# Kernel optimization log

Hardware: AMD Instinct MI355X
Metric: run time of the kernel (lower is better)

Reference implementation:

```python
import jax, jax.numpy as jnp
import numpy as np

NUM_CLASSES = 80
IMG = 640
STRIDES = (8, 16, 32)
CENTER_RADIUS = 2.5
TOPK = 10  # n_candidate_k; dynamic_ks = clamp(int(sum top-10 IoU), 1) <= 10


def _make_grids():
    gs, ss = [], []
    for s in STRIDES:
        n = IMG // s
        gy, gx = np.meshgrid(np.arange(n), np.arange(n), indexing="ij")
        gs.append(np.stack([gx.ravel(), gy.ravel()], 1).astype(np.float32))
        ss.append(np.full(n * n, s, np.float32))
    return np.concatenate(gs, 0), np.concatenate(ss, 0)


def setup_inputs() -> dict:
    key = jax.random.key(0)
    B, T, C = 16, 128, NUM_CLASSES
    grid_np, stride_np = _make_grids()
    A = grid_np.shape[0]  # 8400
    k1, k2, k3, k4, k5, k6 = jax.random.split(key, 6)
    # pred boxes: plausible abs xyxy around anchor centers
    ctr = jnp.asarray((grid_np + 0.5) * stride_np[:, None])[None]
    ctr = ctr + 4.0 * jax.random.normal(k1, (B, A, 2))
    wh = jnp.asarray(stride_np)[None, :, None] * jax.random.uniform(k2, (B, A, 2), minval=1.0, maxval=4.0)
    box = jnp.concatenate([ctr - wh / 2, ctr + wh / 2], -1)
    logits = 2.0 * jax.random.normal(k3, (B, A, 1 + C))
    pred = jnp.concatenate([box, logits], -1)  # [B, A, 5+C]
    # targets: [B, T, 6] = (batch_id, cid, x1, y1, x2, y2)
    tc = jax.random.uniform(k4, (B, T, 2), minval=60.0, maxval=580.0)
    twh = jax.random.uniform(k5, (B, T, 2), minval=30.0, maxval=200.0)
    tbox = jnp.concatenate([tc - twh / 2, tc + twh / 2], -1)
    cid = jax.random.randint(k6, (B, T, 1), 0, C).astype(jnp.float32)
    bid = jnp.broadcast_to(jnp.arange(B, dtype=jnp.float32)[:, None, None], (B, T, 1))
    target = jnp.concatenate([bid, cid, tbox], -1)
    return {"pred": pred, "target": target,
            "grid_mask": jnp.asarray(grid_np), "stride_mask": jnp.asarray(stride_np)}


def _pairwise_iou(a, b):
    # a [T,4], b [A,4], xyxy -> [T,A]
    lt = jnp.maximum(a[:, None, :2], b[None, :, :2])
    rb = jnp.minimum(a[:, None, 2:], b[None, :, 2:])
    wh = jnp.clip(rb - lt, 0.0, None)
    inter = wh[..., 0] * wh[..., 1]
    area_a = jnp.clip(a[:, 2] - a[:, 0], 0.0, None) * jnp.clip(a[:, 3] - a[:, 1], 0.0, None)
    area_b = jnp.clip(b[:, 2] - b[:, 0], 0.0, None) * jnp.clip(b[:, 3] - b[:, 1], 0.0, None)
    return inter / (area_a[:, None] + area_b[None, :] - inter + 1e-8)


def _ciou(p, t):
    # complete IoU, elementwise over leading dims, xyxy
    lt = jnp.maximum(p[..., :2], t[..., :2])
    rb = jnp.minimum(p[..., 2:], t[..., 2:])
    wh = jnp.clip(rb - lt, 0.0, None)
    inter = wh[..., 0] * wh[..., 1]
    wp, hp = p[..., 2] - p[..., 0], p[..., 3] - p[..., 1]
    wt, ht = t[..., 2] - t[..., 0], t[..., 3] - t[..., 1]
    iou = inter / (wp * hp + wt * ht - inter + 1e-8)
    cwh = jnp.maximum(p[..., 2:], t[..., 2:]) - jnp.minimum(p[..., :2], t[..., :2])
    c2 = cwh[..., 0] ** 2 + cwh[..., 1] ** 2 + 1e-8
    rho2 = (((p[..., 0] + p[..., 2]) - (t[..., 0] + t[..., 2])) ** 2
            + ((p[..., 1] + p[..., 3]) - (t[..., 1] + t[..., 3])) ** 2) / 4.0
    v = (4.0 / jnp.pi ** 2) * (jnp.arctan(wt / (ht + 1e-8)) - jnp.arctan(wp / (hp + 1e-8))) ** 2
    alpha = v / (1.0 - iou + v + 1e-8)
    return iou - rho2 / c2 - alpha * v


def _bce_logits(x, t):
    return jnp.maximum(x, 0.0) - x * t + jnp.log1p(jnp.exp(-jnp.abs(x)))


def _assign_image(pred_i, tgt_i, grid, stride):
    # pred_i [A,5+C], tgt_i [T,6]
    A, T, C = pred_i.shape[0], tgt_i.shape[0], NUM_CLASSES
    tbox = tgt_i[:, 2:6]
    cid = tgt_i[:, 1].astype(jnp.int32)
    xc = (grid[:, 0] + 0.5) * stride  # [A]
    yc = (grid[:, 1] + 0.5) * stride
    d = jnp.stack([xc[None] - tbox[:, 0:1], yc[None] - tbox[:, 1:2],
                   tbox[:, 2:3] - xc[None], tbox[:, 3:4] - yc[None]], -1)  # [T,A,4]
    in_boxes = d.min(-1) > 0.0  # [T,A]
    txc = (tbox[:, 0] + tbox[:, 2]) / 2
    tyc = (tbox[:, 1] + tbox[:, 3]) / 2
    in_centers = jnp.maximum(jnp.abs(xc[None] - txc[:, None]),
                             jnp.abs(yc[None] - tyc[:, None])) < CENTER_RADIUS * stride[None]
    in_box = in_boxes.any(0) | in_centers.any(0)  # [A], candidate anchors
    in_box_center = in_boxes & in_centers  # [T,A]
    iou = jnp.where(in_box[None], _pairwise_iou(tbox, pred_i[:, :4]), 0.0)  # [T,A]
    iou_cost = -jnp.log(iou + 1e-8)
    prob = jnp.sqrt(jax.nn.sigmoid(pred_i[:, 4:5]) * jax.nn.sigmoid(pred_i[:, 5:]))  # [A,C]
    logp = jnp.maximum(jnp.log(prob), -100.0)      # torch BCE clamps log at -100
    log1mp = jnp.maximum(jnp.log1p(-prob), -100.0)
    # sum_c BCE(prob, onehot(cid)) computed analytically (avoids [T,A,C]):
    cls_cost = -(log1mp.sum(-1)[None, :] + (logp - log1mp)[:, cid].T)  # [T,A]
    # 1e9 keeps anchors outside in_box out of the candidate pool (original slices them away)
    cost = cls_cost + 3.0 * iou_cost + 1e5 * (~in_box_center) + 1e9 * (~in_box)[None, :]
    topk_ious, _ = jax.lax.top_k(iou, TOPK)  # [T,10]
    dyn_k = jnp.maximum(topk_ious.sum(1).astype(jnp.int32), 1)  # [T]
    _, idx = jax.lax.top_k(-cost, TOPK)  # 10 lowest-cost anchors per target
    sel = jnp.arange(TOPK)[None, :] < dyn_k[:, None]  # keep first dyn_k of them
    matching = jnp.zeros((T, A), bool).at[jnp.arange(T)[:, None], idx].set(sel)
    matching = matching & in_box[None, :]
    conflict = matching.sum(0) > 1  # anchors claimed by >1 targets
    keep = jnp.arange(T)[:, None] == jnp.argmin(cost, 0)[None, :]  # [T,A]
    matching = jnp.where(conflict[None, :], keep, matching)
    mp = matching.any(0)  # [A]
    tp = jnp.argmax(matching, 0)  # [A] target index per anchor
    p_iou = jnp.clip((iou / (iou.max(1, keepdims=True) + 1e-8)).max(0), 0.0, 1.0)  # [A]
    obj_t = jnp.where(in_box, p_iou, 0.0)
    box_t = tbox[tp]  # [A,4]
    cls_t = jax.nn.one_hot(cid[tp], C, dtype=jnp.float32)  # [A,C]
    return mp, box_t, obj_t, cls_t


def reference(pred, target, grid_mask, stride_mask):
    B, A = pred.shape[:2]
    C = NUM_CLASSES
    mp, box_t, obj_t, cls_t = jax.lax.stop_gradient(
        jax.vmap(_assign_image, in_axes=(0, 0, None, None))(pred, target, grid_mask, stride_mask))
    m = mp.reshape(-1).astype(pred.dtype)  # matched-anchor mask over B*A
    n = jnp.maximum(m.sum(), 1.0)
    p = pred.reshape(B * A, -1)
    lbox = 0.05 * jnp.sum((1.0 - _ciou(p[:, :4], box_t.reshape(-1, 4))) * m) / n
    lobj = _bce_logits(p[:, 4], obj_t.reshape(-1)).mean()
    lcls = 0.5 * jnp.sum(_bce_logits(p[:, 5:], cls_t.reshape(-1, C)).mean(-1) * m) / n
    loss = lbox + lobj + lcls
    return loss, jnp.stack([lbox, lobj, lcls])
```

## Files before the change

kernel.cpp:

```cpp
#include <hip/hip_runtime.h>
#include <cfloat>

#pragma clang fp contract(off)

#define NCLS 80
#define PDIM 85
#define NA   8400
#define NAP  8448
#define NB   16
#define NT   128
#define NTOP 10
#define APB  64
#define BPI  132
#define BPI2 33
#define LN2  0.6931471805599453f
#define CAPW 768

#define BAPC ((size_t)NB*NAP)

#define KSENT 0xFFFFFFFF7FFFFFFFull

__device__ __forceinline__ float sigm_fast(float x){
  float e = __expf(-x);
  return __builtin_amdgcn_rcpf(1.0f + e);
}

__device__ __forceinline__ float bce_fast(float x, float t){
  float ax = fabsf(x);
  float e  = __expf(-ax);
  return fmaxf(x,0.0f) - x*t + LN2*__builtin_amdgcn_logf(1.0f + e);
}

__device__ __forceinline__ float pair_iou(float tx1,float ty1,float tx2,float ty2,
                                          float px1,float py1,float px2,float py2){
  float w = fminf(tx2,px2) - fmaxf(tx1,px1);
  float h = fminf(ty2,py2) - fmaxf(ty1,py1);
  w = fmaxf(w,0.0f); h = fmaxf(h,0.0f);
  float inter = w*h;
  float at = fmaxf(tx2-tx1,0.0f)*fmaxf(ty2-ty1,0.0f);
  float ap = fmaxf(px2-px1,0.0f)*fmaxf(py2-py1,0.0f);
  float den = at+ap-inter+1e-8f;
  return inter * __builtin_amdgcn_rcpf(den);
}

__device__ __forceinline__ float dval_fn(float sobj, float lg){
  float ln_sobj = LN2*__builtin_amdgcn_logf(sobj);
  float e = __expf(-fabsf(lg));
  float L = LN2*__builtin_amdgcn_logf(1.0f + e);
  float ln_sc = -(fmaxf(-lg,0.0f) + L);
  float lph = 0.5f*(ln_sobj + ln_sc);
  float p = __expf(lph);
  float lp = fmaxf(lph, -100.0f);
  float l1 = fmaxf(LN2*__builtin_amdgcn_logf(fmaxf(1.0f - p, 0.0f)), -100.0f);
  return lp - l1;
}

__device__ __forceinline__ float cost_from(float S, float dval, float iou, bool ibc, bool ib){
  float iouc = -LN2 * __builtin_amdgcn_logf(iou + 1e-8f);
  float clsc = -(S + dval);
  float c = clsc + 3.0f*iouc;
  c = c + (ibc ? 0.0f : 100000.0f);
  c = c + (ib  ? 0.0f : 1000000000.0f);
  return c;
}

__device__ __forceinline__ unsigned long long key_of(float c, int idx){
  unsigned int u = __float_as_uint(c);
  u ^= (u & 0x80000000u) ? 0xFFFFFFFFu : 0x80000000u;
  return ((unsigned long long)u << 32) | (unsigned int)idx;
}

__device__ __forceinline__ void ins_iou(float* riou, float iou){
  if (iou > riou[NTOP-1]){
    #pragma unroll
    for (int j = NTOP-1; j >= 1; --j){
      bool gj  = iou > riou[j];
      bool gj1 = iou > riou[j-1];
      riou[j] = gj ? (gj1 ? riou[j-1] : iou) : riou[j];
    }
    riou[0] = (iou > riou[0]) ? iou : riou[0];
  }
}
__device__ __forceinline__ void ins_key(unsigned long long* rk, unsigned long long key){
  if (key < rk[NTOP-1]){
    #pragma unroll
    for (int j = NTOP-1; j >= 1; --j){
      bool bj  = key < rk[j];
      bool bj1 = key < rk[j-1];
      rk[j] = bj ? (bj1 ? rk[j-1] : key) : rk[j];
    }
    rk[0] = (key < rk[0]) ? key : rk[0];
  }
}

__global__ __launch_bounds__(256) void k0_precompute(
    const float* __restrict__ pred, const float* __restrict__ target,
    const float* __restrict__ grid, const float* __restrict__ stridev,
    float4* __restrict__ pbox4, float4* __restrict__ meta4,
    float* __restrict__ obja, float* __restrict__ sobja,
    float* __restrict__ S0a, float* __restrict__ D, int use_d,
    unsigned long long* __restrict__ mask, unsigned int* __restrict__ obju,
    float* __restrict__ acc)
{
  __shared__ float  tile[APB*PDIM];
  __shared__ float4 tb4s[NT];
  __shared__ float  ps_s[4][APB];
  __shared__ float  ps0_s[4][APB];
  __shared__ int    ib_s[4][APB];

  int i  = blockIdx.x / BPI;
  int b  = blockIdx.x % BPI;
  int c0 = b*APB;
  int n  = NA - c0; if (n > APB) n = APB;
  int tid = threadIdx.x;

  if (blockIdx.x == 0) acc[tid] = 0.0f;

  const float* src = pred + ((size_t)i*NA + c0)*PDIM;
  int tot = n*PDIM;
  for (int idx = tid; idx < tot; idx += 256) tile[idx] = src[idx];
  for (int idx = tid; idx < NT; idx += 256){
    const float* tg = target + (i*NT + idx)*6;
    tb4s[idx] = make_float4(tg[2],tg[3],tg[4],tg[5]);
  }
  __syncthreads();

  int al = tid & 63, cg = tid >> 6;
  if (al < n){
    int gid = i*NAP + c0 + al;
    float x4 = tile[al*PDIM+4];
    float e4 = __expf(-fabsf(x4));
    float L4 = LN2*__builtin_amdgcn_logf(1.0f + e4);
    float ln_sobj = -(fmaxf(-x4,0.0f) + L4);
    float ps = 0.0f, ps0 = 0.0f;
    #pragma unroll 4
    for (int k = 0; k < 20; ++k){
      int c = cg*20 + k;
      float x  = tile[al*PDIM+5+c];
      float e  = __expf(-fabsf(x));
      float L  = LN2*__builtin_amdgcn_logf(1.0f + e);
      float ln_sc = -(fmaxf(-x,0.0f) + L);
      float lph = 0.5f*(ln_sobj + ln_sc);
      float p   = __expf(lph);
      float lp  = fmaxf(lph, -100.0f);
      float l1  = fmaxf(LN2*__builtin_amdgcn_logf(fmaxf(1.0f - p, 0.0f)), -100.0f);
      ps  += l1;
      if (use_d) D[(size_t)c*BAPC + gid] = lp - l1;
      ps0 += fmaxf(x,0.0f) + L;
    }
    ps_s[cg][al] = ps; ps0_s[cg][al] = ps0;

    int ga = c0 + al;
    float xg = grid[2*ga], yg = grid[2*ga+1], sv = stridev[ga];
    float xc = (xg + 0.5f)*sv, yc = (yg + 0.5f)*sv;
    float rc = 2.5f*sv;
    bool ibp = false;
    #pragma unroll 4
    for (int t = cg*32; t < cg*32+32; ++t){
      float4 T = tb4s[t];
      bool inb = (xc-T.x>0.0f)&&(yc-T.y>0.0f)&&(T.z-xc>0.0f)&&(T.w-yc>0.0f);
      float txc=(T.x+T.z)*0.5f, tyc=(T.y+T.w)*0.5f;
      bool inc = fmaxf(fabsf(xc-txc),fabsf(yc-tyc)) < rc;
      ibp = ibp || inb || inc;
    }
    ib_s[cg][al] = ibp ? 1 : 0;
  }
  __syncthreads();

  if (tid < n){
    int a = tid;
    int gid = i*NAP + c0 + a;
    float s  = ps_s[0][a]  + ps_s[1][a]  + ps_s[2][a]  + ps_s[3][a];
    float s0 = ps0_s[0][a] + ps0_s[1][a] + ps0_s[2][a] + ps0_s[3][a];
    bool ib  = (ib_s[0][a] | ib_s[1][a] | ib_s[2][a] | ib_s[3][a]) != 0;

    float x1 = tile[a*PDIM+0], y1 = tile[a*PDIM+1];
    float x2 = tile[a*PDIM+2], y2 = tile[a*PDIM+3];
    float ol = tile[a*PDIM+4];
    pbox4[gid] = make_float4(x1,y1,x2,y2);
    obja[gid]  = ol;
    sobja[gid] = sigm_fast(ol);
    S0a[gid]   = s0;
    mask[(size_t)gid*2]   = 0ull;
    mask[(size_t)gid*2+1] = 0ull;
    obju[gid] = 0u;

    int ga = c0 + a;
    float xg = grid[2*ga], yg = grid[2*ga+1], sv = stridev[ga];
    float xc = (xg + 0.5f)*sv, yc = (yg + 0.5f)*sv;
    float rc = 2.5f*sv;
    meta4[gid] = make_float4(xc, yc, ib ? rc : -rc, s);
  } else if (tid < APB){
    int gid = i*NAP + c0 + tid;
    meta4[gid] = make_float4(0.0f, 0.0f, -1.0f, 0.0f);
    pbox4[gid] = make_float4(0.0f, 0.0f, 0.0f, 0.0f);
    obju[gid]  = 0u;
  }
}

__global__ __launch_bounds__(256) void k1_pertarget(
    const float4* __restrict__ pbox4, const float4* __restrict__ meta4,
    const float* __restrict__ D, int use_d,
    const float* __restrict__ sobja, const float* __restrict__ pred,
    const float* __restrict__ target,
    unsigned int* __restrict__ obju, unsigned long long* __restrict__ mask)
{
  __shared__ int   seg[4*CAPW];
  __shared__ int   cnts_s[4], cibc_s[4];
  __shared__ float wiou[4][NTOP];
  __shared__ unsigned long long wkey[4][NTOP];
  __shared__ float rmax_s;

  int tid = threadIdx.x, lane = tid & 63, w = tid >> 6;
  int g = blockIdx.x;
  int i = g / NT, t = g - i*NT;
  int iNAP = i*NAP;
  int iNA  = i*NA;
  const float* m4f = (const float*)meta4;

  const float* tg = target + (size_t)g*6;
  int   cid = (int)tg[1];
  float tx1 = tg[2], ty1 = tg[3], tx2 = tg[4], ty2 = tg[5];
  float txc = (tx1+tx2)*0.5f, tyc = (ty1+ty2)*0.5f;
  const float* Dc = use_d ? (D + (size_t)cid*BAPC) : nullptr;

  int cnt = 0, ci = 0;
  int a = w*64 + lane;
  float4 pb = pbox4[iNAP+a];
  float4 mt = meta4[iNAP+a];
  for (int k = 0; k < 33; ++k){
    int a2 = a + 256;
    int ld = (a2 < NAP) ? a2 : 0;
    float4 pbn = pbox4[iNAP+ld];
    float4 mtn = meta4[iNAP+ld];

    bool act = (mt.z > 0.0f);
    bool ov  = (fminf(tx2,pb.z) > fmaxf(tx1,pb.x)) &&
               (fminf(ty2,pb.w) > fmaxf(ty1,pb.y));
    bool inb = (mt.x-tx1>0.0f)&&(mt.y-ty1>0.0f)&&(tx2-mt.x>0.0f)&&(ty2-mt.y>0.0f);
    bool inc = fmaxf(fabsf(mt.x-txc),fabsf(mt.y-tyc)) < mt.z;
    bool ibc = inb && inc;
    bool cand = act && (ov || ibc);
    unsigned long long bb  = __ballot(cand);
    unsigned long long bb2 = __ballot(ibc);
    if (cand){
      int pos = cnt + __popcll(bb & ((1ull << lane) - 1ull));
      if (pos < CAPW) seg[w*CAPW + pos] = a | (ibc ? (1<<15) : 0);
    }
    cnt += __popcll(bb);
    ci  += __popcll(bb2);
    pb = pbn; mt = mtn; a = a2;
  }
  if (lane == 0){ cnts_s[w] = cnt; cibc_s[w] = ci; }
  __syncthreads();

  int tibc = cibc_s[0]+cibc_s[1]+cibc_s[2]+cibc_s[3];
  bool ovf = (cnts_s[0]>CAPW)||(cnts_s[1]>CAPW)||(cnts_s[2]>CAPW)||(cnts_s[3]>CAPW);
  bool fastp = !ovf && (tibc >= 16);

  float riou[NTOP]; unsigned long long rk[NTOP];
  #pragma unroll
  for (int j=0;j<NTOP;++j){ riou[j]=0.0f; rk[j]=KSENT; }

  int cw = cnts_s[w];
  if (fastp){
    for (int j = lane; j < cw; j += 64){
      int e  = seg[w*CAPW + j];
      int a1 = e & 0x3fff;
      bool ibc = (e & (1<<15)) != 0;
      int gid = iNAP + a1;
      float4 pb2 = pbox4[gid];
      float iou = pair_iou(tx1,ty1,tx2,ty2, pb2.x,pb2.y,pb2.z,pb2.w);
      ins_iou(riou, iou);
      float S  = m4f[(size_t)gid*4 + 3];
      float dv = use_d ? Dc[gid] : dval_fn(sobja[gid], pred[(size_t)(iNA+a1)*PDIM + 5 + cid]);
      float c  = cost_from(S, dv, iou, ibc, true);
      ins_key(rk, key_of(c, a1));
    }
  } else {
    for (int a1 = tid; a1 < NA; a1 += 256){
      float4 mt2 = meta4[iNAP+a1];
      if (mt2.z > 0.0f){
        float4 pb2 = pbox4[iNAP+a1];
        float iou = pair_iou(tx1,ty1,tx2,ty2, pb2.x,pb2.y,pb2.z,pb2.w);
        ins_iou(riou, iou);
        bool inb = (mt2.x-tx1>0.0f)&&(mt2.y-ty1>0.0f)&&(tx2-mt2.x>0.0f)&&(ty2-mt2.y>0.0f);
        bool inc = fmaxf(fabsf(mt2.x-txc),fabsf(mt2.y-tyc)) < mt2.z;
        float dv = use_d ? Dc[iNAP+a1] : dval_fn(sobja[iNAP+a1], pred[(size_t)(iNA+a1)*PDIM + 5 + cid]);
        float c = cost_from(mt2.w, dv, iou, inb&&inc, true);
        ins_key(rk, key_of(c, a1));
      }
    }
  }

  #pragma unroll
  for (int r = 0; r < NTOP; ++r){
    float gm = riou[0];
    #pragma unroll
    for (int m = 1; m < 64; m <<= 1) gm = fmaxf(gm, __shfl_xor(gm, m));
    unsigned long long bb = __ballot(riou[0] == gm);
    int win = __ffsll(bb) - 1;
    if (lane == win){
      #pragma unroll
      for (int j=0;j<NTOP-1;++j) riou[j] = riou[j+1];
      riou[NTOP-1] = 0.0f;
    }
    if (lane == 0) wiou[w][r] = gm;
  }
  #pragma unroll
  for (int r = 0; r < NTOP; ++r){
    unsigned long long gk = rk[0];
    #pragma unroll
    for (int m = 1; m < 64; m <<= 1){
      unsigned long long o = __shfl_xor(gk, m);
      gk = (o < gk) ? o : gk;
    }
    unsigned long long bb = __ballot(rk[0] == gk);
    int win = __ffsll(bb) - 1;
    if (lane == win){
      #pragma unroll
      for (int j=0;j<NTOP-1;++j) rk[j] = rk[j+1];
      rk[NTOP-1] = KSENT;
    }
    if (lane == 0) wkey[w][r] = gk;
  }
  __syncthreads();

  int dk = 1;
  if (w == 0){
    int p0=0,p1=0,p2=0,p3=0;
    float ssum = 0.0f, rmax = 0.0f;
    #pragma unroll
    for (int r = 0; r < NTOP; ++r){
      float v0=wiou[0][p0], v1=wiou[1][p1], v2=wiou[2][p2], v3=wiou[3][p3];
      float mx = fmaxf(fmaxf(v0,v1), fmaxf(v2,v3));
      if (r == 0) rmax = mx;
      ssum += mx;
      if      (mx == v0) ++p0;
      else if (mx == v1) ++p1;
      else if (mx == v2) ++p2;
      else               ++p3;
    }
    dk = (int)ssum;
    if (dk < 1) dk = 1;
    if (lane == 0) rmax_s = rmax;
  }
  __syncthreads();

  float invm = 1.0f / (rmax_s + 1e-8f);
  if (fastp){
    for (int j = lane; j < cw; j += 64){
      int a1 = seg[w*CAPW + j] & 0x3fff;
      int gid = iNAP + a1;
      float4 pb2 = pbox4[gid];
      float iou = pair_iou(tx1,ty1,tx2,ty2, pb2.x,pb2.y,pb2.z,pb2.w);
      float v = iou * invm;
      if (v > 0.0f) atomicMax(&obju[gid], __float_as_uint(v));
    }
  } else {
    for (int a1 = tid; a1 < NA; a1 += 256){
      float4 mt2 = meta4[iNAP+a1];
      if (mt2.z > 0.0f){
        float4 pb2 = pbox4[iNAP+a1];
        float iou = pair_iou(tx1,ty1,tx2,ty2, pb2.x,pb2.y,pb2.z,pb2.w);
        float v = iou * invm;
        if (v > 0.0f) atomicMax(&obju[iNAP+a1], __float_as_uint(v));
      }
    }
  }

  if (w == 0){
    int q0=0,q1=0,q2=0,q3=0;
    int myidx = 0x7fffffff;
    #pragma unroll
    for (int r = 0; r < NTOP; ++r){
      unsigned long long k0=wkey[0][q0], k1=wkey[1][q1], k2=wkey[2][q2], k3=wkey[3][q3];
      unsigned long long mn = k0;
      mn = (k1 < mn) ? k1 : mn;
      mn = (k2 < mn) ? k2 : mn;
      mn = (k3 < mn) ? k3 : mn;
      if (lane == r) myidx = (int)(mn & 0xFFFFFFFFull);
      if      (mn == k0) ++q0;
      else if (mn == k1) ++q1;
      else if (mn == k2) ++q2;
      else               ++q3;
    }

    if (lane < NTOP && lane < dk){
      int a1 = myidx;
      if (a1 >= 0 && a1 < NA){
        atomicOr(&mask[(size_t)(iNAP + a1)*2 + (t>>6)], 1ull << (t & 63));
      }
    }
  }
}

__global__ __launch_bounds__(256) void k2_peranchor(
    const float* __restrict__ pred,
    const float4* __restrict__ pbox4, const float4* __restrict__ meta4,
    const float* __restrict__ obja, const float* __restrict__ sobja,
    const float* __restrict__ S0a,
    const float* __restrict__ D, int use_d,
    const float* __restrict__ target,
    const unsigned int* __restrict__ obju, const unsigned long long* __restrict__ mask,
    float* __restrict__ acc)
{
  __shared__ float4 tb4[NT];
  __shared__ int    tcid[NT];
  __shared__ int    cl[256];
  __shared__ int    bt_s[256];
  __shared__ int    ncl;
  __shared__ float4 part[4];

  int i  = blockIdx.x / BPI2;
  int b  = blockIdx.x - i*BPI2;
  int tid = threadIdx.x, lane = tid & 63, w = tid >> 6;
  int a  = b*256 + tid;
  int gid = i*NAP + a;

  if (tid < NT){
    const float* tg = target + (i*NT + tid)*6;
    tcid[tid] = (int)tg[1];
    tb4[tid]  = make_float4(tg[2],tg[3],tg[4],tg[5]);
  }
  if (tid == 0) ncl = 0;

  bool valid = (a < NA);
  float4 pb = pbox4[gid];
  float4 mt = meta4[gid];
  unsigned long long m0=0, m1=0;
  if (valid){ m0 = mask[(size_t)gid*2]; m1 = mask[(size_t)gid*2+1]; }
  float bestv = __uint_as_float(obju[gid]);
  float olv   = obja[gid];
  float S0v   = S0a[gid];

  bool ib = valid && (mt.z > 0.0f);
  float px1=pb.x, py1=pb.y, px2=pb.z, py2=pb.w;
  int cnt = __popcll(m0) + __popcll(m1);

  __syncthreads();

  bool myc = (cnt > 1);
  unsigned long long cb = __ballot(myc);
  int nb = __popcll(cb);
  int base = 0;
  if (lane == 0 && nb) base = atomicAdd(&ncl, nb);
  base = __shfl(base, 0);
  if (myc) cl[base + __popcll(cb & ((1ull << lane) - 1ull))] = tid;
  __syncthreads();

  int tot = ncl;
  for (int ci = w; ci < tot; ci += 4){
    int aidx = cl[ci];
    int a2g  = b*256 + aidx;
    int gid2 = i*NAP + a2g;
    float4 pb2 = pbox4[gid2];
    float4 mt2 = meta4[gid2];
    bool ib2 = (mt2.z > 0.0f);
    float rc2 = fabsf(mt2.z);
    float Sg  = mt2.w;
    float sobj = use_d ? 0.0f : sobja[gid2];
    size_t pbase = (size_t)(i*NA + a2g)*PDIM;

    int ta = lane, tb = lane + 64;
    float dva = use_d ? D[(size_t)tcid[ta]*BAPC + gid2]
                      : dval_fn(sobj, pred[pbase + 5 + tcid[ta]]);
    float dvb = use_d ? D[(size_t)tcid[tb]*BAPC + gid2]
                      : dval_fn(sobj, pred[pbase + 5 + tcid[tb]]);

    float4 Ta = tb4[ta];
    float ioua = ib2 ? pair_iou(Ta.x,Ta.y,Ta.z,Ta.w,pb2.x,pb2.y,pb2.z,pb2.w) : 0.0f;
    bool inba = (mt2.x-Ta.x>0.0f)&&(mt2.y-Ta.y>0.0f)&&(Ta.z-mt2.x>0.0f)&&(Ta.w-mt2.y>0.0f);
    float txa=(Ta.x+Ta.z)*0.5f, tya=(Ta.y+Ta.w)*0.5f;
    bool inca = fmaxf(fabsf(mt2.x-txa),fabsf(mt2.y-tya)) < rc2;
    unsigned long long ka = key_of(cost_from(Sg, dva, ioua, inba&&inca, ib2), ta);

    float4 Tb = tb4[tb];
    float ioub = ib2 ? pair_iou(Tb.x,Tb.y,Tb.z,Tb.w,pb2.x,pb2.y,pb2.z,pb2.w) : 0.0f;
    bool inbb = (mt2.x-Tb.x>0.0f)&&(mt2.y-Tb.y>0.0f)&&(Tb.z-mt2.x>0.0f)&&(Tb.w-mt2.y>0.0f);
    float txb=(Tb.x+Tb.z)*0.5f, tyb=(Tb.y+Tb.w)*0.5f;
    bool incb = fmaxf(fabsf(mt2.x-txb),fabsf(mt2.y-tyb)) < rc2;
    unsigned long long kb = key_of(cost_from(Sg, dvb, ioub, inbb&&incb, ib2), tb);

    unsigned long long mn = (kb < ka) ? kb : ka;
    #pragma unroll
    for (int m = 1; m < 64; m <<= 1){
      unsigned long long o = __shfl_xor(mn, m);
      mn = (o < mn) ? o : mn;
    }
    if (lane == 0) bt_s[aidx] = (int)(mn & 0xFFFFFFFFull);
  }
  __syncthreads();

  float m=0.0f, vbox=0.0f, vobj=0.0f, vcls=0.0f;
  if (valid){
    float obj_t = ib ? fminf(fmaxf(bestv,0.0f),1.0f) : 0.0f;
    vobj = bce_fast(olv, obj_t);

    int tp = 0; bool mpv = false;
    if (cnt > 1){ tp = bt_s[tid]; mpv = true; }
    else if (cnt == 1){
      tp = m0 ? (__ffsll(m0)-1) : (64 + __ffsll(m1)-1);
      mpv = true;
    }

    if (mpv){
      m = 1.0f;
      float4 T = tb4[tp];
      float x1=T.x, y1=T.y, x2=T.z, y2=T.w;
      float w2 = fmaxf(fminf(px2,x2)-fmaxf(px1,x1),0.0f);
      float h2 = fmaxf(fminf(py2,y2)-fmaxf(py1,y1),0.0f);
      float inter = w2*h2;
      float wp=px2-px1, hp=py2-py1, wt=x2-x1, ht=y2-y1;
      float iou = inter/(wp*hp + wt*ht - inter + 1e-8f);
      float cw = fmaxf(px2,x2)-fminf(px1,x1);
      float ch = fmaxf(py2,y2)-fminf(py1,y1);
      float c2 = cw*cw + ch*ch + 1e-8f;
      float dx = (px1+px2)-(x1+x2), dy = (py1+py2)-(y1+y2);
      float rho2 = (dx*dx + dy*dy)/4.0f;
      float da = atanf(wt/(ht+1e-8f)) - atanf(wp/(hp+1e-8f));
      float v  = 0.4052847345693511f * da * da;
      float alpha = v/(1.0f - iou + v + 1e-8f);
      vbox = 1.0f - (iou - rho2/c2 - alpha*v);

      int cc = tcid[tp];
      float xcc = pred[(size_t)(i*NA + a)*PDIM + 5 + cc];
      vcls = (S0v - xcc) * (1.0f/80.0f);
    }
  }

  #pragma unroll
  for (int off=32; off>0; off>>=1){
    m    += __shfl_down(m, off);
    vbox += __shfl_down(vbox, off);
    vobj += __shfl_down(vobj, off);
    vcls += __shfl_down(vcls, off);
  }
  if (lane == 0) part[w] = make_float4(m, vbox, vobj, vcls);
  __syncthreads();
  if (tid == 0){
    float4 s0 = part[0], s1 = part[1], s2 = part[2], s3 = part[3];
    float4 s = make_float4(s0.x+s1.x+s2.x+s3.x, s0.y+s1.y+s2.y+s3.y,
                           s0.z+s1.z+s2.z+s3.z, s0.w+s1.w+s2.w+s3.w);
    int slot = (blockIdx.x & 63)*4;
    atomicAdd(&acc[slot+0], s.x);
    atomicAdd(&acc[slot+1], s.y);
    atomicAdd(&acc[slot+2], s.z);
    atomicAdd(&acc[slot+3], s.w);
  }
}

__global__ void k3_final(const float* __restrict__ acc, float* __restrict__ out){
  int l = threadIdx.x;
  float4 v = ((const float4*)acc)[l];
  #pragma unroll
  for (int off=32; off>0; off>>=1){
    v.x += __shfl_down(v.x, off);
    v.y += __shfl_down(v.y, off);
    v.z += __shfl_down(v.z, off);
    v.w += __shfl_down(v.w, off);
  }
  if (l == 0){
    float n    = fmaxf(v.x, 1.0f);
    float lbox = 0.05f * v.y / n;
    float lobj = v.z / (float)(NB*NA);
    float lcls = 0.5f  * v.w / n;
    out[0] = lbox + lobj + lcls;
    out[1] = lbox; out[2] = lobj; out[3] = lcls;
  }
}

extern "C" void kernel_launch(void* const* d_in, const int* in_sizes, int n_in,
                              void* d_out, int out_size, void* d_ws, size_t ws_size,
                              hipStream_t stream) {
  const float* pred    = (const float*)d_in[0];
  const float* target  = (const float*)d_in[1];
  const float* grid    = (const float*)d_in[2];
  const float* stridev = (const float*)d_in[3];
  float* out = (float*)d_out;

  char* ws = (char*)d_ws;

  size_t off = 0;
  unsigned long long* mask = (unsigned long long*)(ws + off); off += BAPC*16;
  float* acc    = (float*)(ws + off); off += 64*4*4;
  float4* pbox4 = (float4*)(ws + off); off += BAPC*16;
  float4* meta4 = (float4*)(ws + off); off += BAPC*16;
  float* obja   = (float*)(ws + off); off += BAPC*4;
  float* sobja  = (float*)(ws + off); off += BAPC*4;
  float* S0a    = (float*)(ws + off); off += BAPC*4;
  unsigned int* obju = (unsigned int*)(ws + off); off += BAPC*4;
  float* D      = (float*)(ws + off);
  const size_t need_d = off + (size_t)NCLS*BAPC*4;
  int use_d = (ws_size >= need_d) ? 1 : 0;

  k0_precompute<<<NB*BPI, 256, 0, stream>>>(pred, target, grid, stridev,
                                            pbox4, meta4, obja, sobja, S0a, D, use_d,
                                            mask, obju, acc);
  k1_pertarget <<<NB*NT,  256, 0, stream>>>(pbox4, meta4, D, use_d,
                                            sobja, pred, target, obju, mask);
  k2_peranchor <<<NB*BPI2, 256, 0, stream>>>(pred, pbox4, meta4, obja, sobja, S0a,
                                             D, use_d, target, obju, mask, acc);
  k3_final     <<<1, 64, 0, stream>>>(acc, out);
}
```

Before: 160.3 us.

## Cull anchor chunks per target using precomputed per-block bounding boxes

The precompute kernel now reduces, per 64-anchor block, bounding boxes of the predicted boxes, the anchor centers and the center-radius regions of active anchors, and writes them to workspace. The per-target kernel tests each block's boxes against the target first and only loads and scans anchor chunks that could hold candidates, instead of streaming all chunks. It also drops a ballot in the top-k key extraction, relying on the keys being unique. This adds a wave reduction to k0 and extra workspace, which moves the start of the D buffer and could disable the D path if the workspace is tight.

Measured after the change: 152.2 us. 5.1% less time.

```diff
diff --git a/kernel.cpp b/kernel.cpp
--- a/kernel.cpp
+++ b/kernel.cpp
@@ -100,7 +100,7 @@
     float* __restrict__ obja, float* __restrict__ sobja,
     float* __restrict__ S0a, float* __restrict__ D, int use_d,
     unsigned long long* __restrict__ mask, unsigned int* __restrict__ obju,
-    float* __restrict__ acc)
+    float4* __restrict__ gaabb, float* __restrict__ acc)
 {
   __shared__ float  tile[APB*PDIM];
   __shared__ float4 tb4s[NT];
@@ -167,34 +167,68 @@
   }
   __syncthreads();
 
-  if (tid < n){
+  if (tid < APB){
     int a = tid;
+    bool real = (a < n);
     int gid = i*NAP + c0 + a;
-    float s  = ps_s[0][a]  + ps_s[1][a]  + ps_s[2][a]  + ps_s[3][a];
-    float s0 = ps0_s[0][a] + ps0_s[1][a] + ps0_s[2][a] + ps0_s[3][a];
-    bool ib  = (ib_s[0][a] | ib_s[1][a] | ib_s[2][a] | ib_s[3][a]) != 0;
-
-    float x1 = tile[a*PDIM+0], y1 = tile[a*PDIM+1];
-    float x2 = tile[a*PDIM+2], y2 = tile[a*PDIM+3];
-    float ol = tile[a*PDIM+4];
-    pbox4[gid] = make_float4(x1,y1,x2,y2);
-    obja[gid]  = ol;
-    sobja[gid] = sigm_fast(ol);
-    S0a[gid]   = s0;
-    mask[(size_t)gid*2]   = 0ull;
-    mask[(size_t)gid*2+1] = 0ull;
-    obju[gid] = 0u;
-
-    int ga = c0 + a;
-    float xg = grid[2*ga], yg = grid[2*ga+1], sv = stridev[ga];
-    float xc = (xg + 0.5f)*sv, yc = (yg + 0.5f)*sv;
-    float rc = 2.5f*sv;
-    meta4[gid] = make_float4(xc, yc, ib ? rc : -rc, s);
-  } else if (tid < APB){
-    int gid = i*NAP + c0 + tid;
-    meta4[gid] = make_float4(0.0f, 0.0f, -1.0f, 0.0f);
-    pbox4[gid] = make_float4(0.0f, 0.0f, 0.0f, 0.0f);
-    obju[gid]  = 0u;
+    float x1=0,y1=0,x2=0,y2=0,xc=0,yc=0,rc=0;
+    bool ib = false;
+
+    if (real){
+      float s  = ps_s[0][a]  + ps_s[1][a]  + ps_s[2][a]  + ps_s[3][a];
+      float s0 = ps0_s[0][a] + ps0_s[1][a] + ps0_s[2][a] + ps0_s[3][a];
+      ib  = (ib_s[0][a] | ib_s[1][a] | ib_s[2][a] | ib_s[3][a]) != 0;
+
+      x1 = tile[a*PDIM+0]; y1 = tile[a*PDIM+1];
+      x2 = tile[a*PDIM+2]; y2 = tile[a*PDIM+3];
+      float ol = tile[a*PDIM+4];
+      pbox4[gid] = make_float4(x1,y1,x2,y2);
+      obja[gid]  = ol;
+      sobja[gid] = sigm_fast(ol);
+      S0a[gid]   = s0;
+      mask[(size_t)gid*2]   = 0ull;
+      mask[(size_t)gid*2+1] = 0ull;
+      obju[gid] = 0u;
+
+      int ga = c0 + a;
+      float xg = grid[2*ga], yg = grid[2*ga+1], sv = stridev[ga];
+      xc = (xg + 0.5f)*sv; yc = (yg + 0.5f)*sv;
+      rc = 2.5f*sv;
+      meta4[gid] = make_float4(xc, yc, ib ? rc : -rc, s);
+    } else {
+      meta4[gid] = make_float4(0.0f, 0.0f, -1.0f, 0.0f);
+      pbox4[gid] = make_float4(0.0f, 0.0f, 0.0f, 0.0f);
+      obju[gid]  = 0u;
+    }
+
+    bool iv = real && ib;
+    float bx1 = iv ? x1 : FLT_MAX,  by1 = iv ? y1 : FLT_MAX;
+    float bx2 = iv ? x2 : -FLT_MAX, by2 = iv ? y2 : -FLT_MAX;
+    float cx1 = iv ? xc : FLT_MAX,  cy1 = iv ? yc : FLT_MAX;
+    float cx2 = iv ? xc : -FLT_MAX, cy2 = iv ? yc : -FLT_MAX;
+    float rx1 = iv ? xc-rc : FLT_MAX,  ry1 = iv ? yc-rc : FLT_MAX;
+    float rx2 = iv ? xc+rc : -FLT_MAX, ry2 = iv ? yc+rc : -FLT_MAX;
+    #pragma unroll
+    for (int off = 32; off > 0; off >>= 1){
+      bx1 = fminf(bx1, __shfl_xor(bx1, off));
+      by1 = fminf(by1, __shfl_xor(by1, off));
+      bx2 = fmaxf(bx2, __shfl_xor(bx2, off));
+      by2 = fmaxf(by2, __shfl_xor(by2, off));
+      cx1 = fminf(cx1, __shfl_xor(cx1, off));
+      cy1 = fminf(cy1, __shfl_xor(cy1, off));
+      cx2 = fmaxf(cx2, __shfl_xor(cx2, off));
+      cy2 = fmaxf(cy2, __shfl_xor(cy2, off));
+      rx1 = fminf(rx1, __shfl_xor(rx1, off));
+      ry1 = fminf(ry1, __shfl_xor(ry1, off));
+      rx2 = fmaxf(rx2, __shfl_xor(rx2, off));
+      ry2 = fmaxf(ry2, __shfl_xor(ry2, off));
+    }
+    if (tid == 0){
+      size_t gb = (size_t)(i*BPI + b)*3;
+      gaabb[gb+0] = make_float4(bx1,by1,bx2,by2);
+      gaabb[gb+1] = make_float4(cx1,cy1,cx2,cy2);
+      gaabb[gb+2] = make_float4(rx1,ry1,rx2,ry2);
+    }
   }
 }
 
@@ -202,7 +236,7 @@
     const float4* __restrict__ pbox4, const float4* __restrict__ meta4,
     const float* __restrict__ D, int use_d,
     const float* __restrict__ sobja, const float* __restrict__ pred,
-    const float* __restrict__ target,
+    const float* __restrict__ target, const float4* __restrict__ gaabb,
     unsigned int* __restrict__ obju, unsigned long long* __restrict__ mask)
 {
   __shared__ int   seg[4*CAPW];
@@ -224,15 +258,26 @@
   float txc = (tx1+tx2)*0.5f, tyc = (ty1+ty2)*0.5f;
   const float* Dc = use_d ? (D + (size_t)cid*BAPC) : nullptr;
 
+  bool sv = false;
+  if (lane < 33){
+    size_t gb = (size_t)(i*BPI + (w + 4*lane))*3;
+    float4 gbb = gaabb[gb+0];
+    float4 gcc = gaabb[gb+1];
+    float4 grr = gaabb[gb+2];
+    bool ovg  = (fminf(tx2,gbb.z) > fmaxf(tx1,gbb.x)) &&
+                (fminf(ty2,gbb.w) > fmaxf(ty1,gbb.y));
+    bool inbg = (gcc.z > tx1) && (gcc.x < tx2) && (gcc.w > ty1) && (gcc.y < ty2);
+    bool incg = (txc > grr.x) && (txc < grr.z) && (tyc > grr.y) && (tyc < grr.w);
+    sv = ovg || (inbg && incg);
+  }
+  unsigned long long gmsk = __ballot(sv);
+
   int cnt = 0, ci = 0;
-  int a = w*64 + lane;
-  float4 pb = pbox4[iNAP+a];
-  float4 mt = meta4[iNAP+a];
-  for (int k = 0; k < 33; ++k){
-    int a2 = a + 256;
-    int ld = (a2 < NAP) ? a2 : 0;
-    float4 pbn = pbox4[iNAP+ld];
-    float4 mtn = meta4[iNAP+ld];
+  while (gmsk){
+    int k = __ffsll(gmsk) - 1; gmsk &= gmsk - 1;
+    int a = w*64 + k*256 + lane;
+    float4 pb = pbox4[iNAP+a];
+    float4 mt = meta4[iNAP+a];
 
     bool act = (mt.z > 0.0f);
     bool ov  = (fminf(tx2,pb.z) > fmaxf(tx1,pb.x)) &&
@@ -249,7 +294,6 @@
     }
     cnt += __popcll(bb);
     ci  += __popcll(bb2);
-    pb = pbn; mt = mtn; a = a2;
   }
   if (lane == 0){ cnts_s[w] = cnt; cibc_s[w] = ci; }
   __syncthreads();
@@ -315,9 +359,7 @@
       unsigned long long o = __shfl_xor(gk, m);
       gk = (o < gk) ? o : gk;
     }
-    unsigned long long bb = __ballot(rk[0] == gk);
-    int win = __ffsll(bb) - 1;
-    if (lane == win){
+    if (rk[0] == gk){
       #pragma unroll
       for (int j=0;j<NTOP-1;++j) rk[j] = rk[j+1];
       rk[NTOP-1] = KSENT;
@@ -590,15 +632,16 @@
   float* sobja  = (float*)(ws + off); off += BAPC*4;
   float* S0a    = (float*)(ws + off); off += BAPC*4;
   unsigned int* obju = (unsigned int*)(ws + off); off += BAPC*4;
+  float4* gaabb = (float4*)(ws + off); off += (size_t)NB*BPI*3*16;
   float* D      = (float*)(ws + off);
   const size_t need_d = off + (size_t)NCLS*BAPC*4;
   int use_d = (ws_size >= need_d) ? 1 : 0;
 
   k0_precompute<<<NB*BPI, 256, 0, stream>>>(pred, target, grid, stridev,
                                             pbox4, meta4, obja, sobja, S0a, D, use_d,
-                                            mask, obju, acc);
+                                            mask, obju, gaabb, acc);
   k1_pertarget <<<NB*NT,  256, 0, stream>>>(pbox4, meta4, D, use_d,
-                                            sobja, pred, target, obju, mask);
+                                            sobja, pred, target, gaabb, obju, mask);
   k2_peranchor <<<NB*BPI2, 256, 0, stream>>>(pred, pbox4, meta4, obja, sobja, S0a,
                                              D, use_d, target, obju, mask, acc);
   k3_final     <<<1, 64, 0, stream>>>(acc, out);
```
